# Kernel tuning notes

Hardware: AMD Instinct MI355X
Metric: run time of the kernel (lower is better)

Reference implementation:

```python
import math
import jax, jax.numpy as jnp
import numpy as np

B, D, K = 512, 512, 93431
S_SCALE = 64.0
MARGIN = 0.5
EPS = 0.1
COS_M = math.cos(MARGIN)
SIN_M = math.sin(MARGIN)
THRESHOLD = math.cos(math.pi - MARGIN)
MM = math.sin(math.pi - MARGIN) * MARGIN


def setup_inputs() -> dict:
    key = jax.random.key(0)
    k1, k2, k3 = jax.random.split(key, 3)
    x = jax.random.normal(k1, (B, D), dtype=jnp.float32)
    label = jax.random.randint(k2, (B,), 0, K, dtype=jnp.int64)
    kernel = jax.random.normal(k3, (D, K), dtype=jnp.float32) * 0.01
    t = jnp.zeros((1,), dtype=jnp.float32)
    return {"x": x, "label": label, "kernel": kernel, "t": t}


def reference(x, label, kernel, t):
    # L2-normalize embeddings (rows) and kernel (columns), cosine logits
    xn = x / jnp.linalg.norm(x, axis=1, keepdims=True)
    kn = kernel / jnp.linalg.norm(kernel, axis=0, keepdims=True)
    cos_theta = jnp.clip(xn @ kn, -1.0, 1.0)  # [B, K]

    rows = jnp.arange(B)
    target_logit = cos_theta[rows, label]  # [B]
    sin_theta = jnp.sqrt(1.0 - target_logit ** 2)
    cos_theta_m = target_logit * COS_M - sin_theta * SIN_M  # [B]

    mask = cos_theta > cos_theta_m[:, None]  # [B, K]
    final_target_logit = jnp.where(target_logit > THRESHOLD,
                                   cos_theta_m, target_logit - MM)

    # buffer update runs under no_grad in torch; updated t is used immediately
    t_new = jax.lax.stop_gradient(target_logit.mean() * 0.01 + 0.99 * t[0])

    # hard-example re-weighting, then scatter margin logit at the label column
    ct = jnp.where(mask, cos_theta * (t_new + cos_theta), cos_theta)
    ct = ct.at[rows, label].set(final_target_logit)
    logits = ct * S_SCALE

    # label-smoothed cross-entropy without materializing the one-hot matrix
    logp = jax.nn.log_softmax(logits, axis=1)  # [B, K]
    nll = (1.0 - EPS) * logp[rows, label] + (EPS / K) * logp.sum(axis=1)
    loss = -nll.mean()
    return loss
```

## Files before the change

kernel.cpp:

```cpp
#include <hip/hip_runtime.h>
#include <math.h>

#define BB 512
#define DD 512
#define KK 93431
#define KPAD 93440

#define S_SCALEf 64.0f
#define COS_Mf   0.87758256189037276f
#define SIN_Mf   0.47942553860420301f
#define THRESHf (-0.87758256189037276f)
#define MMf      0.23971276930210151f
#define EPSf     0.1f
#define MFIXf    65.0f

#define KSCALE 64.0f
#define XSCALE 16.0f
#define INV_KX (1.0f / (KSCALE * XSCALE))

typedef float f32x4 __attribute__((ext_vector_type(4)));
typedef long  l64x2 __attribute__((ext_vector_type(2)));

__device__ __forceinline__ unsigned short f2bf(float f) {
    union { float f; unsigned u; } v; v.f = f;
    unsigned r = v.u + 0x7FFFu + ((v.u >> 16) & 1u);
    return (unsigned short)(r >> 16);
}

__device__ __forceinline__ unsigned pack4_fp8(float a, float b, float c, float d) {
    unsigned v = 0;
    v = __builtin_amdgcn_cvt_pk_fp8_f32(a, b, v, false);
    v = __builtin_amdgcn_cvt_pk_fp8_f32(c, d, v, true);
    return v;
}

__device__ __forceinline__ void gload16(const void* g, void* l) {
    __builtin_amdgcn_global_load_lds(
        (const __attribute__((address_space(1))) unsigned int*)g,
        (__attribute__((address_space(3))) unsigned int*)l, 16, 0, 0);
}

__global__ void rownorm_k(const float* __restrict__ x, float* __restrict__ xn,
                          unsigned char* __restrict__ xnf8) {
    int b = blockIdx.x;
    int t = threadIdx.x;
    float v0 = x[b * DD + t];
    float v1 = x[b * DD + t + 256];
    float ss = v0 * v0 + v1 * v1;
    for (int off = 32; off; off >>= 1) ss += __shfl_down(ss, off);
    __shared__ float wred[4];
    __shared__ float s_inv;
    __shared__ float rbF[512];
    if ((t & 63) == 0) wred[t >> 6] = ss;
    __syncthreads();
    if (t == 0) s_inv = rsqrtf(wred[0] + wred[1] + wred[2] + wred[3]);
    __syncthreads();
    float inv = s_inv;
    float a0 = v0 * inv, a1 = v1 * inv;
    xn[b * DD + t]       = a0;
    xn[b * DD + t + 256] = a1;
    rbF[t]       = a0;
    rbF[t + 256] = a1;
    __syncthreads();
    if (t < 64) {
        int kt = t >> 3, ch = t & 7;
        float v[8];
#pragma unroll
        for (int e = 0; e < 8; ++e) v[e] = XSCALE * rbF[kt * 64 + ch * 8 + e];
        unsigned w0 = pack4_fp8(v[0], v[1], v[2], v[3]);
        unsigned w1 = pack4_fp8(v[4], v[5], v[6], v[7]);
        uint2 o = {w0, w1};
        int off = (ch < 4) ? ch * 16 : (ch - 4) * 16 + 8;
        *reinterpret_cast<uint2*>(&xnf8[(size_t)b * DD + kt * 64 + off]) = o;
    }
}

__global__ __launch_bounds__(256) void tcvt_k(const float* __restrict__ ker,
                                              unsigned char* __restrict__ kerf8,
                                              float* __restrict__ ssq) {
    __shared__ float tile[64][65];
    __shared__ float sp[256];
    int t = threadIdx.x;
    int c0 = blockIdx.x * 64;
    int kt = blockIdx.y;
    int d0 = kt * 64;
    int lc = t & 63;
    int dq = t >> 6;
    int gc = c0 + lc;
    bool valid = gc < KK;
    float ss = 0.f;
#pragma unroll
    for (int i = 0; i < 16; ++i) {
        int d = dq + i * 4;
        float v = valid ? ker[(size_t)(d0 + d) * KK + gc] : 0.f;
        tile[d][lc] = v;
        ss = fmaf(v, v, ss);
    }
    sp[t] = ss;
    __syncthreads();
    if (t < 64 && (c0 + t) < KK) {
        float tot = sp[t] + sp[t + 64] + sp[t + 128] + sp[t + 192];
        atomicAdd(&ssq[c0 + t], tot);
    }
#pragma unroll
    for (int j = 0; j < 2; ++j) {
        int l = t + 256 * j;
        int c = l >> 3;
        int ch = l & 7;
        float v[8];
#pragma unroll
        for (int e = 0; e < 8; ++e) v[e] = KSCALE * tile[ch * 8 + e][c];
        unsigned w0 = pack4_fp8(v[0], v[1], v[2], v[3]);
        unsigned w1 = pack4_fp8(v[4], v[5], v[6], v[7]);
        uint2 o = {w0, w1};
        int off = (ch < 4) ? ch * 16 : (ch - 4) * 16 + 8;
        *reinterpret_cast<uint2*>(&kerf8[(size_t)(c0 + c) * DD + kt * 64 + off]) = o;
    }
}

__global__ void target_k(const float* __restrict__ xn, const float* __restrict__ ker,
                         const float* __restrict__ ssq, const int* __restrict__ label,
                         float* __restrict__ tl) {
    int b = blockIdx.x;
    int lane = threadIdx.x;
    int col = label[b];
    float acc = 0.f;
#pragma unroll
    for (int d = lane; d < DD; d += 64)
        acc = fmaf(xn[b * DD + d], ker[(size_t)d * KK + col], acc);
    for (int off = 32; off; off >>= 1) acc += __shfl_down(acc, off);
    if (lane == 0) {
        float c = acc * rsqrtf(ssq[col]);
        c = fminf(1.f, fmaxf(-1.f, c));
        tl[b] = c;
    }
}

__global__ void scalar_k(const float* __restrict__ tl, const float* __restrict__ t_in,
                         float* __restrict__ ctm, float* __restrict__ ftl,
                         float* __restrict__ tnew, float* __restrict__ ssq) {
    int t = threadIdx.x;
    float v = tl[t];
    __shared__ float red[8];
    __shared__ float s_tn;
    float s = v;
    for (int off = 32; off; off >>= 1) s += __shfl_down(s, off);
    if ((t & 63) == 0) red[t >> 6] = s;
    __syncthreads();
    if (t == 0) {
        float tot = 0.f;
        for (int i = 0; i < 8; ++i) tot += red[i];
        s_tn = (tot / 512.0f) * 0.01f + 0.99f * t_in[0];
        tnew[0] = s_tn;
    }
    __syncthreads();
    float st = sqrtf(fmaxf(0.f, 1.f - v * v));
    float cm = v * COS_Mf - st * SIN_Mf;
    ctm[t] = cm;
    ftl[t] = (v > THRESHf) ? cm : (v - MMf);
    if (t < KPAD - KK) ssq[KK + t] = 1.f;
}

#define TMt 128
#define TNt 128
#define NWG ((KPAD / TNt) * (BB / TMt))

__global__ __launch_bounds__(256, 4) void gemm_k(
    const unsigned char* __restrict__ xnf8,
    const unsigned char* __restrict__ kerf8,
    const float* __restrict__ ssq,
    const int* __restrict__ label,
    const float* __restrict__ ctm, const float* __restrict__ ftl,
    const float* __restrict__ tnew,
    float* __restrict__ gse, float* __restrict__ gsl)
{
    __shared__ __align__(16) unsigned char As[2][TMt * 64];
    __shared__ __align__(16) unsigned char Bs[2][TNt * 64];
    __shared__ float se_s[TMt], sl_s[TMt], ctm_s[TMt], ftl_s[TMt];
    __shared__ int   lbl_s[TMt];

    int wg = blockIdx.x;
    int id = (wg & 7) * (NWG / 8) + (wg >> 3);
    int by = id & 3;
    int bx = id >> 2;
    int row0 = by * TMt;
    int col0 = bx * TNt;

    const int t = threadIdx.x;
    const int lane = t & 63;
    const int w = t >> 6;
    const int wm = w >> 1;
    const int wn = w & 1;
    const int cp0 = lane & 15;
    const int kq = lane >> 4;

    if (t < TMt) {
        se_s[t] = 0.f; sl_s[t] = 0.f;
        int r = row0 + t;
        ctm_s[t] = ctm[r]; ftl_s[t] = ftl[r]; lbl_s[t] = label[r];
    }
    const float tn = tnew[0];

    float sq4[4];
#pragma unroll
    for (int fc = 0; fc < 4; ++fc)
        sq4[fc] = ssq[col0 + wn * 64 + fc * 16 + cp0];

#define STAGE(ktv, bi)                                                         \
    {                                                                          \
        _Pragma("unroll")                                                      \
        for (int j = 0; j < 2; ++j) {                                          \
            const int l = t + 256 * j;                                         \
            const int r = l >> 2, s = l & 3;                                   \
            const int ss2 = s ^ ((r >> 1) & 3);                                \
            gload16(&xnf8[(size_t)(row0 + r) * DD + (ktv) * 64 + ss2 * 16],    \
                    (void*)&As[bi][l * 16]);                                   \
        }                                                                      \
        _Pragma("unroll")                                                      \
        for (int j = 0; j < 2; ++j) {                                          \
            const int l = t + 256 * j;                                         \
            const int r = l >> 2, s = l & 3;                                   \
            const int ss2 = s ^ ((r >> 1) & 3);                                \
            gload16(&kerf8[(size_t)(col0 + r) * DD + (ktv) * 64 + ss2 * 16],   \
                    (void*)&Bs[bi][l * 16]);                                   \
        }                                                                      \
    }

    f32x4 acc[4][4];
#pragma unroll
    for (int fm = 0; fm < 4; ++fm)
#pragma unroll
        for (int fc = 0; fc < 4; ++fc) acc[fm][fc] = (f32x4)0.f;

    STAGE(0, 0);
    __builtin_amdgcn_sched_barrier(0);
    asm volatile("s_waitcnt vmcnt(0)" ::: "memory");
    __builtin_amdgcn_s_barrier();

#pragma unroll
    for (int kt = 0; kt < 8; ++kt) {
        const int bi = kt & 1;
        if (kt < 7) STAGE(kt + 1, bi ^ 1);
        const char* Ap = (const char*)&As[bi][0];
        const char* Bp = (const char*)&Bs[bi][0];

        l64x2 bv[4];
#pragma unroll
        for (int fc = 0; fc < 4; ++fc) {
            const int ct = wn * 64 + fc * 16 + cp0;
            bv[fc] = *reinterpret_cast<const l64x2*>(
                Bp + ct * 64 + ((kq ^ ((ct >> 1) & 3)) * 16));
        }
        __builtin_amdgcn_s_setprio(1);
#pragma unroll
        for (int fm = 0; fm < 4; ++fm) {
            const int rt = wm * 64 + fm * 16 + cp0;
            l64x2 av = *reinterpret_cast<const l64x2*>(
                Ap + rt * 64 + ((kq ^ ((rt >> 1) & 3)) * 16));
#pragma unroll
            for (int fc = 0; fc < 4; ++fc) {
                acc[fm][fc] = __builtin_amdgcn_mfma_f32_16x16x32_fp8_fp8(
                    av[0], bv[fc][0], acc[fm][fc], 0, 0, 0);
                acc[fm][fc] = __builtin_amdgcn_mfma_f32_16x16x32_fp8_fp8(
                    av[1], bv[fc][1], acc[fm][fc], 0, 0, 0);
            }
        }
        __builtin_amdgcn_s_setprio(0);

        __builtin_amdgcn_sched_barrier(0);
        asm volatile("s_waitcnt vmcnt(0)" ::: "memory");
        __builtin_amdgcn_s_barrier();
    }
#undef STAGE

    float inv4[4];
#pragma unroll
    for (int fc = 0; fc < 4; ++fc) inv4[fc] = rsqrtf(sq4[fc]) * INV_KX;

#pragma unroll
    for (int fm = 0; fm < 4; ++fm) {
#pragma unroll
        for (int reg = 0; reg < 4; ++reg) {
            const int rt = wm * 64 + fm * 16 + (kq << 2) + reg;
            float cm = ctm_s[rt], ft = ftl_s[rt];
            const int rel = lbl_s[rt] - (col0 + wn * 64 + cp0);
            float se = 0.f, sl = 0.f;
#pragma unroll
            for (int fc = 0; fc < 4; ++fc) {
                float c = acc[fm][fc][reg] * inv4[fc];
                c = fminf(1.f, fmaxf(-1.f, c));
                float v = (c > cm) ? c * (tn + c) : c;
                if (rel == fc * 16) v = ft;
                float lg = S_SCALEf * v;
                se += __expf(lg - MFIXf);
                sl += lg;
            }
#pragma unroll
            for (int off = 8; off; off >>= 1) {
                se += __shfl_down(se, off, 16);
                sl += __shfl_down(sl, off, 16);
            }
            if (cp0 == 0) {
                atomicAdd(&se_s[rt], se);
                atomicAdd(&sl_s[rt], sl);
            }
        }
    }
    __syncthreads();
    if (t < TMt) {
        atomicAdd(&gse[row0 + t], se_s[t]);
        atomicAdd(&gsl[row0 + t], sl_s[t]);
    }
}

__global__ void loss_k(const float* __restrict__ gse, const float* __restrict__ gsl,
                       const float* __restrict__ ftl, float* __restrict__ out) {
    int t = threadIdx.x;
    float lse = MFIXf + logf(gse[t]);
    float lbl_logit = S_SCALEf * ftl[t];
    float nll = (1.f - EPSf) * (lbl_logit - lse)
              + (EPSf / (float)KK) * (gsl[t] - (float)KK * lse);
    __shared__ float red[8];
    float s = nll;
    for (int off = 32; off; off >>= 1) s += __shfl_down(s, off);
    if ((t & 63) == 0) red[t >> 6] = s;
    __syncthreads();
    if (t == 0) {
        float tot = 0.f;
        for (int i = 0; i < 8; ++i) tot += red[i];
        out[0] = -(tot / 512.0f);
    }
}

extern "C" void kernel_launch(void* const* d_in, const int* in_sizes, int n_in,
                              void* d_out, int out_size, void* d_ws, size_t ws_size,
                              hipStream_t stream) {
    const float* x     = (const float*)d_in[0];
    const int*   label = (const int*)d_in[1];
    const float* ker   = (const float*)d_in[2];
    const float* t_in  = (const float*)d_in[3];
    float* out = (float*)d_out;

    float* ws   = (float*)d_ws;
    float* xn   = ws;
    float* ssq  = xn + 262144;
    float* gse  = ssq + KPAD;
    float* gsl  = gse + 512;
    float* tl   = gsl + 512;
    float* ctm  = tl + 512;
    float* ftl  = ctm + 512;
    float* tnew = ftl + 512;
    unsigned char* xnf8  = (unsigned char*)(tnew + 64);
    unsigned char* kerf8 = xnf8 + (size_t)512 * 512;

    hipMemsetAsync(ssq, 0, (KPAD + 1024) * sizeof(float), stream);

    rownorm_k<<<BB, 256, 0, stream>>>(x, xn, xnf8);
    tcvt_k<<<dim3(KPAD / 64, DD / 64), 256, 0, stream>>>(ker, kerf8, ssq);
    target_k<<<BB, 64, 0, stream>>>(xn, ker, ssq, label, tl);
    scalar_k<<<1, 512, 0, stream>>>(tl, t_in, ctm, ftl, tnew, ssq);
    gemm_k<<<NWG, 256, 0, stream>>>(xnf8, kerf8, ssq, label, ctm, ftl, tnew, gse, gsl);
    loss_k<<<1, 512, 0, stream>>>(gse, gsl, ftl, out);
}
```

Measured before the change: 125.9 us.

## Quantize embeddings and kernel to FP4 and use scaled 16x16x128 MFMA

Replaces the FP8 quantization of normalized embeddings and class weights with a software FP4 (e2m1) quantizer that packs eight values per 32-bit word. The GEMM now uses the MX-scaled f8f6f4 MFMA with FP4 operands and unit block scales, halving the K-loop iterations and the bytes staged through LDS. Pre-scaling factors are doubled to make better use of the FP4 range. The goal is to cut GEMM memory traffic and MFMA issue count. The cost is a large loss of precision in the cosine logits, plus a branchy per-element conversion in the transpose kernel.

After: 184.7 us. +46.7%, slower.

```diff
diff --git a/kernel.cpp b/kernel.cpp
--- a/kernel.cpp
+++ b/kernel.cpp
@@ -14,24 +14,28 @@
 #define EPSf     0.1f
 #define MFIXf    65.0f
 
-#define KSCALE 64.0f
-#define XSCALE 16.0f
+#define KSCALE 128.0f
+#define XSCALE 32.0f
 #define INV_KX (1.0f / (KSCALE * XSCALE))
+#define SCALE1 0x7F7F7F7F
 
 typedef float f32x4 __attribute__((ext_vector_type(4)));
-typedef long  l64x2 __attribute__((ext_vector_type(2)));
-
-__device__ __forceinline__ unsigned short f2bf(float f) {
-    union { float f; unsigned u; } v; v.f = f;
-    unsigned r = v.u + 0x7FFFu + ((v.u >> 16) & 1u);
-    return (unsigned short)(r >> 16);
-}
-
-__device__ __forceinline__ unsigned pack4_fp8(float a, float b, float c, float d) {
-    unsigned v = 0;
-    v = __builtin_amdgcn_cvt_pk_fp8_f32(a, b, v, false);
-    v = __builtin_amdgcn_cvt_pk_fp8_f32(c, d, v, true);
-    return v;
+typedef int   i32x4 __attribute__((ext_vector_type(4)));
+typedef int   i32x8 __attribute__((ext_vector_type(8)));
+
+__device__ __forceinline__ unsigned q_fp4(float v) {
+    unsigned s = (__float_as_uint(v) >> 31) << 3;
+    float a = fabsf(v);
+    unsigned c;
+    if      (a < 0.25f) c = 0;
+    else if (a < 0.75f) c = 1;
+    else if (a < 1.25f) c = 2;
+    else if (a < 1.75f) c = 3;
+    else if (a < 2.50f) c = 4;
+    else if (a < 3.50f) c = 5;
+    else if (a < 5.00f) c = 6;
+    else                c = 7;
+    return s | c;
 }
 
 __device__ __forceinline__ void gload16(const void* g, void* l) {
@@ -41,7 +45,7 @@
 }
 
 __global__ void rownorm_k(const float* __restrict__ x, float* __restrict__ xn,
-                          unsigned char* __restrict__ xnf8) {
+                          unsigned int* __restrict__ xnf4) {
     int b = blockIdx.x;
     int t = threadIdx.x;
     float v0 = x[b * DD + t];
@@ -63,20 +67,16 @@
     rbF[t + 256] = a1;
     __syncthreads();
     if (t < 64) {
-        int kt = t >> 3, ch = t & 7;
-        float v[8];
-#pragma unroll
-        for (int e = 0; e < 8; ++e) v[e] = XSCALE * rbF[kt * 64 + ch * 8 + e];
-        unsigned w0 = pack4_fp8(v[0], v[1], v[2], v[3]);
-        unsigned w1 = pack4_fp8(v[4], v[5], v[6], v[7]);
-        uint2 o = {w0, w1};
-        int off = (ch < 4) ? ch * 16 : (ch - 4) * 16 + 8;
-        *reinterpret_cast<uint2*>(&xnf8[(size_t)b * DD + kt * 64 + off]) = o;
+        unsigned v = 0;
+#pragma unroll
+        for (int e = 0; e < 8; ++e)
+            v |= q_fp4(XSCALE * rbF[t * 8 + e]) << (4 * e);
+        xnf4[b * 64 + t] = v;
     }
 }
 
 __global__ __launch_bounds__(256) void tcvt_k(const float* __restrict__ ker,
-                                              unsigned char* __restrict__ kerf8,
+                                              unsigned int* __restrict__ kerf4,
                                               float* __restrict__ ssq) {
     __shared__ float tile[64][65];
     __shared__ float sp[256];
@@ -107,14 +107,11 @@
         int l = t + 256 * j;
         int c = l >> 3;
         int ch = l & 7;
-        float v[8];
-#pragma unroll
-        for (int e = 0; e < 8; ++e) v[e] = KSCALE * tile[ch * 8 + e][c];
-        unsigned w0 = pack4_fp8(v[0], v[1], v[2], v[3]);
-        unsigned w1 = pack4_fp8(v[4], v[5], v[6], v[7]);
-        uint2 o = {w0, w1};
-        int off = (ch < 4) ? ch * 16 : (ch - 4) * 16 + 8;
-        *reinterpret_cast<uint2*>(&kerf8[(size_t)(c0 + c) * DD + kt * 64 + off]) = o;
+        unsigned v = 0;
+#pragma unroll
+        for (int e = 0; e < 8; ++e)
+            v |= q_fp4(KSCALE * tile[ch * 8 + e][c]) << (4 * e);
+        kerf4[(size_t)(c0 + c) * 64 + kt * 8 + ch] = v;
     }
 }
 
@@ -166,8 +163,8 @@
 #define NWG ((KPAD / TNt) * (BB / TMt))
 
 __global__ __launch_bounds__(256, 4) void gemm_k(
-    const unsigned char* __restrict__ xnf8,
-    const unsigned char* __restrict__ kerf8,
+    const unsigned char* __restrict__ xnf4,
+    const unsigned char* __restrict__ kerf4,
     const float* __restrict__ ssq,
     const int* __restrict__ label,
     const float* __restrict__ ctm, const float* __restrict__ ftl,
@@ -213,7 +210,7 @@
             const int l = t + 256 * j;                                         \
             const int r = l >> 2, s = l & 3;                                   \
             const int ss2 = s ^ ((r >> 1) & 3);                                \
-            gload16(&xnf8[(size_t)(row0 + r) * DD + (ktv) * 64 + ss2 * 16],    \
+            gload16(&xnf4[(size_t)(row0 + r) * 256 + (ktv) * 64 + ss2 * 16],   \
                     (void*)&As[bi][l * 16]);                                   \
         }                                                                      \
         _Pragma("unroll")                                                      \
@@ -221,7 +218,7 @@
             const int l = t + 256 * j;                                         \
             const int r = l >> 2, s = l & 3;                                   \
             const int ss2 = s ^ ((r >> 1) & 3);                                \
-            gload16(&kerf8[(size_t)(col0 + r) * DD + (ktv) * 64 + ss2 * 16],   \
+            gload16(&kerf4[(size_t)(col0 + r) * 256 + (ktv) * 64 + ss2 * 16],  \
                     (void*)&Bs[bi][l * 16]);                                   \
         }                                                                      \
     }
@@ -238,32 +235,33 @@
     __builtin_amdgcn_s_barrier();
 
 #pragma unroll
-    for (int kt = 0; kt < 8; ++kt) {
+    for (int kt = 0; kt < 4; ++kt) {
         const int bi = kt & 1;
-        if (kt < 7) STAGE(kt + 1, bi ^ 1);
+        if (kt < 3) STAGE(kt + 1, bi ^ 1);
         const char* Ap = (const char*)&As[bi][0];
         const char* Bp = (const char*)&Bs[bi][0];
 
-        l64x2 bv[4];
+        i32x8 bop[4];
 #pragma unroll
         for (int fc = 0; fc < 4; ++fc) {
             const int ct = wn * 64 + fc * 16 + cp0;
-            bv[fc] = *reinterpret_cast<const l64x2*>(
+            i32x4 bd = *reinterpret_cast<const i32x4*>(
                 Bp + ct * 64 + ((kq ^ ((ct >> 1) & 3)) * 16));
+            bop[fc] = (i32x8){bd[0], bd[1], bd[2], bd[3], 0, 0, 0, 0};
         }
         __builtin_amdgcn_s_setprio(1);
 #pragma unroll
         for (int fm = 0; fm < 4; ++fm) {
             const int rt = wm * 64 + fm * 16 + cp0;
-            l64x2 av = *reinterpret_cast<const l64x2*>(
+            i32x4 ad = *reinterpret_cast<const i32x4*>(
                 Ap + rt * 64 + ((kq ^ ((rt >> 1) & 3)) * 16));
-#pragma unroll
-            for (int fc = 0; fc < 4; ++fc) {
-                acc[fm][fc] = __builtin_amdgcn_mfma_f32_16x16x32_fp8_fp8(
-                    av[0], bv[fc][0], acc[fm][fc], 0, 0, 0);
-                acc[fm][fc] = __builtin_amdgcn_mfma_f32_16x16x32_fp8_fp8(
-                    av[1], bv[fc][1], acc[fm][fc], 0, 0, 0);
-            }
+            i32x8 aop = (i32x8){ad[0], ad[1], ad[2], ad[3], 0, 0, 0, 0};
+#pragma unroll
+            for (int fc = 0; fc < 4; ++fc)
+                acc[fm][fc] = __builtin_amdgcn_mfma_scale_f32_16x16x128_f8f6f4(
+                    aop, bop[fc], acc[fm][fc],
+                    4 , 4 ,
+                    0, SCALE1, 0, SCALE1);
         }
         __builtin_amdgcn_s_setprio(0);
 
@@ -350,15 +348,17 @@
     float* ctm  = tl + 512;
     float* ftl  = ctm + 512;
     float* tnew = ftl + 512;
-    unsigned char* xnf8  = (unsigned char*)(tnew + 64);
-    unsigned char* kerf8 = xnf8 + (size_t)512 * 512;
+    unsigned int* xnf4  = (unsigned int*)(tnew + 64);
+    unsigned int* kerf4 = xnf4 + (size_t)512 * 64;
 
     hipMemsetAsync(ssq, 0, (KPAD + 1024) * sizeof(float), stream);
 
-    rownorm_k<<<BB, 256, 0, stream>>>(x, xn, xnf8);
-    tcvt_k<<<dim3(KPAD / 64, DD / 64), 256, 0, stream>>>(ker, kerf8, ssq);
+    rownorm_k<<<BB, 256, 0, stream>>>(x, xn, xnf4);
+    tcvt_k<<<dim3(KPAD / 64, DD / 64), 256, 0, stream>>>(ker, kerf4, ssq);
     target_k<<<BB, 64, 0, stream>>>(xn, ker, ssq, label, tl);
     scalar_k<<<1, 512, 0, stream>>>(tl, t_in, ctm, ftl, tnew, ssq);
-    gemm_k<<<NWG, 256, 0, stream>>>(xnf8, kerf8, ssq, label, ctm, ftl, tnew, gse, gsl);
+    gemm_k<<<NWG, 256, 0, stream>>>((const unsigned char*)xnf4,
+                                    (const unsigned char*)kerf4,
+                                    ssq, label, ctm, ftl, tnew, gse, gsl);
     loss_k<<<1, 512, 0, stream>>>(gse, gsl, ftl, out);
 }
```

## Use three-stage LDS pipeline with 32-byte K tiles and natural fp8 layout

Applied to the files above, without the earlier changes.

The GEMM's shared-memory pipeline changes from double buffering of 64-byte K slices to triple buffering of 32-byte K slices. Partial vmcnt waits keep two tiles of global loads in flight. The fp8 packing of x and kernel now writes contiguous 8-byte chunks instead of the interleaved layout, and the LDS swizzle and fragment reads are adjusted to match. This is meant to hide more global load latency with a smaller per-stage LDS footprint. The cost is twice as many barriers and iterations, each with half as much MFMA work between syncs.

Result: slower. 140.9 us (+11.9%).

```diff
diff --git a/kernel.cpp b/kernel.cpp
--- a/kernel.cpp
+++ b/kernel.cpp
@@ -19,13 +19,6 @@
 #define INV_KX (1.0f / (KSCALE * XSCALE))
 
 typedef float f32x4 __attribute__((ext_vector_type(4)));
-typedef long  l64x2 __attribute__((ext_vector_type(2)));
-
-__device__ __forceinline__ unsigned short f2bf(float f) {
-    union { float f; unsigned u; } v; v.f = f;
-    unsigned r = v.u + 0x7FFFu + ((v.u >> 16) & 1u);
-    return (unsigned short)(r >> 16);
-}
 
 __device__ __forceinline__ unsigned pack4_fp8(float a, float b, float c, float d) {
     unsigned v = 0;
@@ -63,15 +56,12 @@
     rbF[t + 256] = a1;
     __syncthreads();
     if (t < 64) {
-        int kt = t >> 3, ch = t & 7;
         float v[8];
 #pragma unroll
-        for (int e = 0; e < 8; ++e) v[e] = XSCALE * rbF[kt * 64 + ch * 8 + e];
-        unsigned w0 = pack4_fp8(v[0], v[1], v[2], v[3]);
-        unsigned w1 = pack4_fp8(v[4], v[5], v[6], v[7]);
-        uint2 o = {w0, w1};
-        int off = (ch < 4) ? ch * 16 : (ch - 4) * 16 + 8;
-        *reinterpret_cast<uint2*>(&xnf8[(size_t)b * DD + kt * 64 + off]) = o;
+        for (int e = 0; e < 8; ++e) v[e] = XSCALE * rbF[t * 8 + e];
+        uint2 o = { pack4_fp8(v[0], v[1], v[2], v[3]),
+                    pack4_fp8(v[4], v[5], v[6], v[7]) };
+        *reinterpret_cast<uint2*>(&xnf8[(size_t)b * DD + t * 8]) = o;
     }
 }
 
@@ -82,8 +72,7 @@
     __shared__ float sp[256];
     int t = threadIdx.x;
     int c0 = blockIdx.x * 64;
-    int kt = blockIdx.y;
-    int d0 = kt * 64;
+    int d0 = blockIdx.y * 64;
     int lc = t & 63;
     int dq = t >> 6;
     int gc = c0 + lc;
@@ -110,11 +99,9 @@
         float v[8];
 #pragma unroll
         for (int e = 0; e < 8; ++e) v[e] = KSCALE * tile[ch * 8 + e][c];
-        unsigned w0 = pack4_fp8(v[0], v[1], v[2], v[3]);
-        unsigned w1 = pack4_fp8(v[4], v[5], v[6], v[7]);
-        uint2 o = {w0, w1};
-        int off = (ch < 4) ? ch * 16 : (ch - 4) * 16 + 8;
-        *reinterpret_cast<uint2*>(&kerf8[(size_t)(c0 + c) * DD + kt * 64 + off]) = o;
+        uint2 o = { pack4_fp8(v[0], v[1], v[2], v[3]),
+                    pack4_fp8(v[4], v[5], v[6], v[7]) };
+        *reinterpret_cast<uint2*>(&kerf8[(size_t)(c0 + c) * DD + d0 + ch * 8]) = o;
     }
 }
 
@@ -174,8 +161,8 @@
     const float* __restrict__ tnew,
     float* __restrict__ gse, float* __restrict__ gsl)
 {
-    __shared__ __align__(16) unsigned char As[2][TMt * 64];
-    __shared__ __align__(16) unsigned char Bs[2][TNt * 64];
+    __shared__ __align__(16) unsigned char As[3][TMt * 32];
+    __shared__ __align__(16) unsigned char Bs[3][TNt * 32];
     __shared__ float se_s[TMt], sl_s[TMt], ctm_s[TMt], ftl_s[TMt];
     __shared__ int   lbl_s[TMt];
 
@@ -208,22 +195,12 @@
 
 #define STAGE(ktv, bi)                                                         \
     {                                                                          \
-        _Pragma("unroll")                                                      \
-        for (int j = 0; j < 2; ++j) {                                          \
-            const int l = t + 256 * j;                                         \
-            const int r = l >> 2, s = l & 3;                                   \
-            const int ss2 = s ^ ((r >> 1) & 3);                                \
-            gload16(&xnf8[(size_t)(row0 + r) * DD + (ktv) * 64 + ss2 * 16],    \
-                    (void*)&As[bi][l * 16]);                                   \
-        }                                                                      \
-        _Pragma("unroll")                                                      \
-        for (int j = 0; j < 2; ++j) {                                          \
-            const int l = t + 256 * j;                                         \
-            const int r = l >> 2, s = l & 3;                                   \
-            const int ss2 = s ^ ((r >> 1) & 3);                                \
-            gload16(&kerf8[(size_t)(col0 + r) * DD + (ktv) * 64 + ss2 * 16],   \
-                    (void*)&Bs[bi][l * 16]);                                   \
-        }                                                                      \
+        const int r = t >> 1, p = t & 1;                                       \
+        const int sc = p ^ ((r >> 2) & 1);                                     \
+        gload16(&xnf8[(size_t)(row0 + r) * DD + (ktv) * 32 + sc * 16],         \
+                (void*)&As[bi][t * 16]);                                       \
+        gload16(&kerf8[(size_t)(col0 + r) * DD + (ktv) * 32 + sc * 16],        \
+                (void*)&Bs[bi][t * 16]);                                       \
     }
 
     f32x4 acc[4][4];
@@ -233,43 +210,46 @@
         for (int fc = 0; fc < 4; ++fc) acc[fm][fc] = (f32x4)0.f;
 
     STAGE(0, 0);
+    STAGE(1, 1);
     __builtin_amdgcn_sched_barrier(0);
-    asm volatile("s_waitcnt vmcnt(0)" ::: "memory");
+    asm volatile("s_waitcnt vmcnt(2)" ::: "memory");
     __builtin_amdgcn_s_barrier();
 
 #pragma unroll
-    for (int kt = 0; kt < 8; ++kt) {
-        const int bi = kt & 1;
-        if (kt < 7) STAGE(kt + 1, bi ^ 1);
+    for (int kt = 0; kt < 16; ++kt) {
+        const int bi = kt % 3;
+        if (kt + 2 < 16) STAGE(kt + 2, (kt + 2) % 3);
         const char* Ap = (const char*)&As[bi][0];
         const char* Bp = (const char*)&Bs[bi][0];
 
-        l64x2 bv[4];
+        long bfr[4];
 #pragma unroll
         for (int fc = 0; fc < 4; ++fc) {
             const int ct = wn * 64 + fc * 16 + cp0;
-            bv[fc] = *reinterpret_cast<const l64x2*>(
-                Bp + ct * 64 + ((kq ^ ((ct >> 1) & 3)) * 16));
+            bfr[fc] = *reinterpret_cast<const long*>(
+                Bp + ct * 32 + (((kq >> 1) ^ ((ct >> 2) & 1)) * 16) + (kq & 1) * 8);
         }
         __builtin_amdgcn_s_setprio(1);
 #pragma unroll
         for (int fm = 0; fm < 4; ++fm) {
             const int rt = wm * 64 + fm * 16 + cp0;
-            l64x2 av = *reinterpret_cast<const l64x2*>(
-                Ap + rt * 64 + ((kq ^ ((rt >> 1) & 3)) * 16));
-#pragma unroll
-            for (int fc = 0; fc < 4; ++fc) {
+            long af = *reinterpret_cast<const long*>(
+                Ap + rt * 32 + (((kq >> 1) ^ ((rt >> 2) & 1)) * 16) + (kq & 1) * 8);
+#pragma unroll
+            for (int fc = 0; fc < 4; ++fc)
                 acc[fm][fc] = __builtin_amdgcn_mfma_f32_16x16x32_fp8_fp8(
-                    av[0], bv[fc][0], acc[fm][fc], 0, 0, 0);
-                acc[fm][fc] = __builtin_amdgcn_mfma_f32_16x16x32_fp8_fp8(
-                    av[1], bv[fc][1], acc[fm][fc], 0, 0, 0);
-            }
+                    af, bfr[fc], acc[fm][fc], 0, 0, 0);
         }
         __builtin_amdgcn_s_setprio(0);
 
-        __builtin_amdgcn_sched_barrier(0);
-        asm volatile("s_waitcnt vmcnt(0)" ::: "memory");
-        __builtin_amdgcn_s_barrier();
+        if (kt + 1 < 16) {
+            __builtin_amdgcn_sched_barrier(0);
+            if (kt + 2 < 16)
+                asm volatile("s_waitcnt vmcnt(2)" ::: "memory");
+            else
+                asm volatile("s_waitcnt vmcnt(0)" ::: "memory");
+            __builtin_amdgcn_s_barrier();
+        }
     }
 #undef STAGE
 
```
